# Kernel tuning notes

Hardware: AMD Instinct MI355X
Metric: run time of the kernel (lower is better)

The kernel has to match this reference:

```python
import jax, jax.numpy as jnp
import numpy as np

N_HEADS = 8
HEAD_DIM = 64
SCALE = HEAD_DIM ** -0.5


def setup_inputs() -> dict:
    key = jax.random.key(0)
    k1, k2, k3 = jax.random.split(key, 3)
    B, C, Hs, Ws = 8, 512, 64, 64
    x = jax.random.normal(k1, (B, C, Hs, Ws), dtype=jnp.float32)
    _h = jnp.zeros((1,), dtype=jnp.int32)  # unused arg in original forward
    # proj_in: Linear(C, 3*H*hd); stored as (in, out) so y = x @ W + b
    W_in = jax.random.normal(k2, (C, 3 * N_HEADS * HEAD_DIM), dtype=jnp.float32) * (C ** -0.5)
    b_in = jnp.zeros((3 * N_HEADS * HEAD_DIM,), dtype=jnp.float32)
    W_out = jax.random.normal(k3, (N_HEADS * HEAD_DIM, C), dtype=jnp.float32) * ((N_HEADS * HEAD_DIM) ** -0.5)
    b_out = jnp.zeros((C,), dtype=jnp.float32)
    return {"x": x, "_h": _h, "W_in": W_in, "b_in": b_in, "W_out": W_out, "b_out": b_out}


def reference(x, _h, W_in, b_in, W_out, b_out):
    in_shape = x.shape
    B, C = in_shape[0], in_shape[1]
    # (B, C, *spatial) -> (B, S, C)
    xf = x.reshape(B, C, -1).transpose(0, 2, 1)
    S = xf.shape[1]
    # fused QKV projection -> (B, S, H, 3*hd), chunk into q, k, v: (B, S, H, hd)
    qkv = (xf @ W_in + b_in).reshape(B, S, N_HEADS, 3 * HEAD_DIM)
    q, k, v = jnp.split(qkv, 3, axis=-1)
    # NOTE: faithful to the original, SDPA receives (B, S, H, hd) WITHOUT a
    # transpose to (B, H, S, hd): attention runs over the heads axis (HxH),
    # batched over (B, S).
    scores = jnp.einsum("bsqd,bskd->bsqk", q, k) * SCALE  # (B, S, H, H)
    attn = jax.nn.softmax(scores, axis=-1)
    out = jnp.einsum("bsqk,bskd->bsqd", attn, v)  # (B, S, H, hd)
    out = out.reshape(B, S, N_HEADS * HEAD_DIM)
    out = out @ W_out + b_out  # (B, S, C)
    return out.transpose(0, 2, 1).reshape(in_shape)
```

## Files before the change

### kernel.cpp

```cpp
#include <hip/hip_runtime.h>
#include <hip/hip_bf16.h>

typedef __attribute__((ext_vector_type(8))) short bh8;
typedef __attribute__((ext_vector_type(4))) float fx4;

#define GLOAD16(g, l)                                                          \
  __builtin_amdgcn_global_load_lds(                                            \
      (const __attribute__((address_space(1))) void*)(g),                      \
      (__attribute__((address_space(3))) void*)(l), 16, 0, 0)

__device__ __forceinline__ unsigned short f2bf(float f) {
  unsigned int u = __float_as_uint(f);
  u += 0x7fffu + ((u >> 16) & 1u);
  return (unsigned short)(u >> 16);
}
__device__ __forceinline__ float bf2f(short h) {
  return __uint_as_float(((unsigned int)(unsigned short)h) << 16);
}

__global__ __launch_bounds__(256) void transpose_cvt(
    const float* __restrict__ in, short* __restrict__ out, int R, int Ccols) {
  __shared__ float tile[64][65];
  const int b = blockIdx.z;
  const int c0 = blockIdx.x * 64;
  const int r0 = blockIdx.y * 64;
  const float* ip = in + (size_t)b * R * Ccols;
  short* op = out + (size_t)b * Ccols * R;
  const int tx = threadIdx.x & 63, ty = threadIdx.x >> 6;
#pragma unroll
  for (int i = 0; i < 16; ++i) {
    int r = ty + i * 4;
    tile[tx][r] = ip[(size_t)(r0 + r) * Ccols + c0 + tx];
  }
  __syncthreads();
#pragma unroll
  for (int i = 0; i < 16; ++i) {
    int cc = ty + i * 4;
    op[(size_t)(c0 + cc) * R + r0 + tx] = (short)f2bf(tile[cc][tx]);
  }
}

template <int MODE>
__global__ __launch_bounds__(256) void gemm_bt(
    const short* __restrict__ A, const short* __restrict__ Bt,
    const float* __restrict__ bias, void* __restrict__ Cout,
    int M, int N, int K, int tok0) {
  __shared__ short As[128 * 32] __attribute__((aligned(16)));
  __shared__ short Bs[128 * 32] __attribute__((aligned(16)));
  const int tid = threadIdx.x;
  const int lane = tid & 63;
  const int wv = tid >> 6;
  const int wr = wv >> 1, wc = wv & 1;
  const int m0 = blockIdx.y * 128, n0 = blockIdx.x * 128;

  const int lr = lane & 15;
  const int lk = (lane >> 4) * 8;

  fx4 acc[4][4] = {};

  const int srow = tid >> 2;
  const int skoff = (tid & 3) * 8;
  const size_t abase = (size_t)(m0 + srow) * K + skoff;
  const size_t bbase = (size_t)(n0 + srow) * K + skoff;
  char* lA0 = (char*)As + wv * 1024;
  char* lA1 = (char*)As + 4096 + wv * 1024;
  char* lB0 = (char*)Bs + wv * 1024;
  char* lB1 = (char*)Bs + 4096 + wv * 1024;

  for (int k0 = 0; k0 < K; k0 += 32) {
    if (k0) __syncthreads();
    GLOAD16(A + abase + k0, lA0);
    GLOAD16(A + abase + (size_t)64 * K + k0, lA1);
    GLOAD16(Bt + bbase + k0, lB0);
    GLOAD16(Bt + bbase + (size_t)64 * K + k0, lB1);
    __syncthreads();

    bh8 af[4], bfm[4];
#pragma unroll
    for (int i = 0; i < 4; ++i) {
      af[i] = *(const bh8*)&As[(wr * 64 + i * 16 + lr) * 32 + lk];
      bfm[i] = *(const bh8*)&Bs[(wc * 64 + i * 16 + lr) * 32 + lk];
    }
#pragma unroll
    for (int i = 0; i < 4; ++i)
#pragma unroll
      for (int j = 0; j < 4; ++j)
        acc[i][j] = __builtin_amdgcn_mfma_f32_16x16x32_bf16(af[i], bfm[j],
                                                            acc[i][j], 0, 0, 0);
  }

  if (MODE == 1) {
    short* C = (short*)Cout;
#pragma unroll
    for (int i = 0; i < 4; ++i) {
      const int gm = m0 + wr * 64 + i * 16 + (lane >> 4) * 4;
#pragma unroll
      for (int j = 0; j < 4; ++j) {
        const int gn = n0 + wc * 64 + j * 16 + lr;
        const float bv = bias[gn];
#pragma unroll
        for (int r = 0; r < 4; ++r)
          C[(size_t)(gm + r) * N + gn] = (short)f2bf(acc[i][j][r] + bv);
      }
    }
  } else {
    float* C = (float*)Cout;
#pragma unroll
    for (int i = 0; i < 4; ++i) {
      const int ch0 = m0 + wr * 64 + i * 16 + (lane >> 4) * 4;
#pragma unroll
      for (int j = 0; j < 4; ++j) {
        const int t = tok0 + n0 + wc * 64 + j * 16 + lr;
        const int bb = t >> 12, s = t & 4095;
#pragma unroll
        for (int r = 0; r < 4; ++r) {
          const int ch = ch0 + r;
          C[((size_t)(bb * 512 + ch)) * 4096 + s] = acc[i][j][r] + bias[ch];
        }
      }
    }
  }
}

__global__ __launch_bounds__(256) void attn_kernel(
    const short* __restrict__ QKV, short* __restrict__ AO) {
  __shared__ short sq[4][1536] __attribute__((aligned(16)));
  const int tid = threadIdx.x, lane = tid & 63, wv = tid >> 6;
  const int t = blockIdx.x * 4 + wv;

  {
    const short* g = QKV + (size_t)t * 1536 + lane * 8;
    char* l = (char*)&sq[wv][0];
    GLOAD16(g, l);
    GLOAD16(g + 512, l + 1024);
    GLOAD16(g + 1024, l + 2048);
  }
  asm volatile("s_waitcnt vmcnt(0)" ::: "memory");

  const int i = lane >> 3, j = lane & 7;
  const short* q = &sq[wv][i * 192];
  const short* k = &sq[wv][j * 192 + 64];
  float s = 0.f;
#pragma unroll
  for (int c = 0; c < 8; ++c) {
    bh8 qa = *(const bh8*)&q[c * 8];
    bh8 ka = *(const bh8*)&k[c * 8];
#pragma unroll
    for (int e = 0; e < 8; ++e) s += bf2f(qa[e]) * bf2f(ka[e]);
  }
  s *= 0.125f;

  float m = s;
  m = fmaxf(m, __shfl_xor(m, 1));
  m = fmaxf(m, __shfl_xor(m, 2));
  m = fmaxf(m, __shfl_xor(m, 4));
  float p = __expf(s - m);
  float sum = p;
  sum += __shfl_xor(sum, 1);
  sum += __shfl_xor(sum, 2);
  sum += __shfl_xor(sum, 4);
  const float a = p / sum;

  float o[8] = {};
#pragma unroll
  for (int jj = 0; jj < 8; ++jj) {
    const float aj = __shfl(a, (lane & 56) | jj);
    bh8 va = *(const bh8*)&sq[wv][jj * 192 + 128 + j * 8];
#pragma unroll
    for (int e = 0; e < 8; ++e) o[e] += aj * bf2f(va[e]);
  }
  bh8 ov;
#pragma unroll
  for (int e = 0; e < 8; ++e) ov[e] = (short)f2bf(o[e]);
  *(bh8*)&AO[(size_t)t * 512 + i * 64 + j * 8] = ov;
}

extern "C" void kernel_launch(void* const* d_in, const int* in_sizes, int n_in,
                              void* d_out, int out_size, void* d_ws,
                              size_t ws_size, hipStream_t stream) {
  const float* x = (const float*)d_in[0];
  const float* W_in = (const float*)d_in[2];
  const float* b_in = (const float*)d_in[3];
  const float* W_out = (const float*)d_in[4];
  const float* b_out = (const float*)d_in[5];
  float* out = (float*)d_out;

  short* Xbf = (short*)d_ws;
  short* WinT = Xbf + (size_t)32768 * 512;
  short* WoutT = WinT + (size_t)1536 * 512;
  short* QKVc = WoutT + (size_t)512 * 512;

  const size_t fixed_bytes =
      ((size_t)32768 * 512 + (size_t)1536 * 512 + (size_t)512 * 512) * 2;
  int NC = 1;
  while (NC < 256 &&
         fixed_bytes + ((size_t)32768 / NC) * 1536 * 2 > ws_size)
    NC <<= 1;
  const int Mc = 32768 / NC;

  transpose_cvt<<<dim3(64, 8, 8), 256, 0, stream>>>(x, Xbf, 512, 4096);
  transpose_cvt<<<dim3(24, 8, 1), 256, 0, stream>>>(W_in, WinT, 512, 1536);
  transpose_cvt<<<dim3(8, 8, 1), 256, 0, stream>>>(W_out, WoutT, 512, 512);

  for (int c = 0; c < NC; ++c) {
    const int t0 = c * Mc;
    short* Ach = Xbf + (size_t)t0 * 512;
    gemm_bt<1><<<dim3(12, Mc / 128), 256, 0, stream>>>(Ach, WinT, b_in, QKVc,
                                                       Mc, 1536, 512, 0);
    attn_kernel<<<dim3(Mc / 4), 256, 0, stream>>>(QKVc, Ach);
    gemm_bt<2><<<dim3(Mc / 128, 4), 256, 0, stream>>>(WoutT, Ach, b_out, out,
                                                      512, Mc, 512, t0);
  }
}
```

Before: 267.0 us.

## Double-buffer GEMM LDS tiles and remap workgroups for locality

The GEMM now keeps two LDS buffers for A and B, so the global-to-LDS load of the next K tile is issued before the MFMA work on the current tile, cutting one barrier per iteration. It also remaps workgroup IDs with an 8-way interleave and a mode-dependent traversal order, aiming to improve L2 or cache reuse across neighbouring blocks. LDS use doubles, which may lower occupancy. The loop relies on the single barrier per iteration, with s_waitcnt inserted by the compiler, to order the async loads safely.

Result: faster. 255.8 us (-4.2%).

```diff
diff --git a/kernel.cpp b/kernel.cpp
--- a/kernel.cpp
+++ b/kernel.cpp
@@ -45,13 +45,30 @@
     const short* __restrict__ A, const short* __restrict__ Bt,
     const float* __restrict__ bias, void* __restrict__ Cout,
     int M, int N, int K, int tok0) {
-  __shared__ short As[128 * 32] __attribute__((aligned(16)));
-  __shared__ short Bs[128 * 32] __attribute__((aligned(16)));
+  __shared__ short As[2][128 * 32] __attribute__((aligned(16)));
+  __shared__ short Bs[2][128 * 32] __attribute__((aligned(16)));
   const int tid = threadIdx.x;
   const int lane = tid & 63;
   const int wv = tid >> 6;
   const int wr = wv >> 1, wc = wv & 1;
-  const int m0 = blockIdx.y * 128, n0 = blockIdx.x * 128;
+
+  const int nbx = gridDim.x, nby = gridDim.y;
+  const int nwg = nbx * nby;
+  int h = blockIdx.y * nbx + blockIdx.x;
+  int L = h;
+  if ((nwg & 7) == 0) {
+    const int q = nwg >> 3;
+    L = (h & 7) * q + (h >> 3);
+  }
+  int bx, by;
+  if (MODE == 1) {
+    by = L / nbx;
+    bx = L - by * nbx;
+  } else {
+    bx = L / nby;
+    by = L - bx * nby;
+  }
+  const int m0 = by * 128, n0 = bx * 128;
 
   const int lr = lane & 15;
   const int lk = (lane >> 4) * 8;
@@ -62,24 +79,34 @@
   const int skoff = (tid & 3) * 8;
   const size_t abase = (size_t)(m0 + srow) * K + skoff;
   const size_t bbase = (size_t)(n0 + srow) * K + skoff;
-  char* lA0 = (char*)As + wv * 1024;
-  char* lA1 = (char*)As + 4096 + wv * 1024;
-  char* lB0 = (char*)Bs + wv * 1024;
-  char* lB1 = (char*)Bs + 4096 + wv * 1024;
-
+  const int ldoff = wv * 1024;
+
+  {
+    char* lA = (char*)As[0] + ldoff;
+    char* lB = (char*)Bs[0] + ldoff;
+    GLOAD16(A + abase, lA);
+    GLOAD16(A + abase + (size_t)64 * K, lA + 4096);
+    GLOAD16(Bt + bbase, lB);
+    GLOAD16(Bt + bbase + (size_t)64 * K, lB + 4096);
+  }
+  __syncthreads();
+
+  int cur = 0;
   for (int k0 = 0; k0 < K; k0 += 32) {
-    if (k0) __syncthreads();
-    GLOAD16(A + abase + k0, lA0);
-    GLOAD16(A + abase + (size_t)64 * K + k0, lA1);
-    GLOAD16(Bt + bbase + k0, lB0);
-    GLOAD16(Bt + bbase + (size_t)64 * K + k0, lB1);
-    __syncthreads();
+    if (k0 + 32 < K) {
+      char* lA = (char*)As[cur ^ 1] + ldoff;
+      char* lB = (char*)Bs[cur ^ 1] + ldoff;
+      GLOAD16(A + abase + k0 + 32, lA);
+      GLOAD16(A + abase + (size_t)64 * K + k0 + 32, lA + 4096);
+      GLOAD16(Bt + bbase + k0 + 32, lB);
+      GLOAD16(Bt + bbase + (size_t)64 * K + k0 + 32, lB + 4096);
+    }
 
     bh8 af[4], bfm[4];
 #pragma unroll
     for (int i = 0; i < 4; ++i) {
-      af[i] = *(const bh8*)&As[(wr * 64 + i * 16 + lr) * 32 + lk];
-      bfm[i] = *(const bh8*)&Bs[(wc * 64 + i * 16 + lr) * 32 + lk];
+      af[i] = *(const bh8*)&As[cur][(wr * 64 + i * 16 + lr) * 32 + lk];
+      bfm[i] = *(const bh8*)&Bs[cur][(wc * 64 + i * 16 + lr) * 32 + lk];
     }
 #pragma unroll
     for (int i = 0; i < 4; ++i)
@@ -87,6 +114,9 @@
       for (int j = 0; j < 4; ++j)
         acc[i][j] = __builtin_amdgcn_mfma_f32_16x16x32_bf16(af[i], bfm[j],
                                                             acc[i][j], 0, 0, 0);
+
+    __syncthreads();
+    cur ^= 1;
   }
 
   if (MODE == 1) {
```
